# Performance work log

Measured on AMD Instinct MI355X. Metric: run time of the kernel, lower is better.

The kernel has to match this reference:

```python
import jax, jax.numpy as jnp
import numpy as np

B, T, D = 2, 4096, 1024
EI, N, DTR, K = 2048, 16, 64, 4  # d_inner, d_state, dt_rank, d_conv


def setup_inputs() -> dict:
    key = jax.random.key(0)
    ks = jax.random.split(key, 12)
    s = lambda k, shape, sc=0.02: jax.random.normal(k, shape, jnp.float32) * sc
    return dict(
        x=jax.random.normal(ks[0], (B, T, D), jnp.float32),
        W=s(ks[1], (B, D, D), 0.02),
        norm_w=jnp.ones((D,), jnp.float32),
        in_proj=s(ks[2], (2 * EI, D)),
        conv_w=s(ks[3], (EI, 1, K), 0.1),
        conv_b=jnp.zeros((EI,), jnp.float32),
        x_proj=s(ks[4], (DTR + 2 * N, EI)),
        dt_proj_w=s(ks[5], (EI, DTR), 0.1),
        dt_proj_b=jnp.full((EI,), -4.6, jnp.float32),  # softplus -> ~0.01 init dt
        A_log=jnp.log(jnp.tile(jnp.arange(1, N + 1, dtype=jnp.float32), (EI, 1))),
        D_param=jnp.ones((EI,), jnp.float32),
        out_proj=s(ks[6], (D, EI)),
        proj_write=s(ks[7], (D, D)),
        proj_read=s(ks[8], (D, D)),
        decay=jnp.float32(4.6),
    )


def _rmsnorm(x, w):
    return x * jax.lax.rsqrt(jnp.mean(x * x, axis=-1, keepdims=True) + 1e-6) * w


def _mamba(x, in_proj, conv_w, conv_b, x_proj, dt_proj_w, dt_proj_b, A_log, D_param, out_proj):
    # x: [B,T,D]
    xz = jnp.einsum('btd,ed->bte', x, in_proj)          # [B,T,2*EI]
    xp, z = jnp.split(xz, 2, axis=-1)
    # depthwise causal conv over time
    xc = jax.lax.conv_general_dilated(
        xp.transpose(0, 2, 1), conv_w, (1,), [(K - 1, 0)],
        dimension_numbers=('NCH', 'OIH', 'NCH'), feature_group_count=EI)
    xc = jax.nn.silu(xc.transpose(0, 2, 1) + conv_b)     # [B,T,EI]
    dbl = jnp.einsum('bte,fe->btf', xc, x_proj)          # [B,T,DTR+2N]
    dt = jax.nn.softplus(jnp.einsum('btr,er->bte', dbl[..., :DTR], dt_proj_w) + dt_proj_b)
    Bs = dbl[..., DTR:DTR + N]                           # [B,T,N]
    Cs = dbl[..., DTR + N:]                              # [B,T,N]
    A = -jnp.exp(A_log)                                  # [EI,N]

    def step(h, inp):
        dt_t, u_t, B_t, C_t = inp                        # [B,EI],[B,EI],[B,N],[B,N]
        dA = jnp.exp(dt_t[..., None] * A)                # [B,EI,N]
        h = dA * h + (dt_t * u_t)[..., None] * B_t[:, None, :]
        y = jnp.einsum('ben,bn->be', h, C_t)
        return h, y

    h0 = jnp.zeros((x.shape[0], EI, N), x.dtype)
    _, ys = jax.lax.scan(step, h0, (dt.transpose(1, 0, 2), xc.transpose(1, 0, 2),
                                    Bs.transpose(1, 0, 2), Cs.transpose(1, 0, 2)))
    y = ys.transpose(1, 0, 2) + xc * D_param
    y = y * jax.nn.silu(z)
    return jnp.einsum('bte,de->btd', y, out_proj)


def _memory_attend(out, W, proj_write, proj_read, decay):
    Bn, Tn, Dn = out.shape
    log_gamma = jnp.log(jax.nn.sigmoid(decay))
    v = jnp.einsum('btd,ed->bte', out, proj_write)       # [B,T,D]
    wk = jnp.pad(out[:, :-1], ((0, 0), (1, 0), (0, 0)))  # shift-right keys
    rk = out
    pos = jnp.arange(Tn)
    diffs = jnp.clip(pos[:, None] - 1 - pos[None, :], 0, None)
    M = jnp.exp(diffs * log_gamma) * (pos[:, None] > pos[None, :])  # [T,T] decay mask
    scores = jnp.einsum('btd,bsd->bts', rk, wk) * M      # [B,T,T]
    reads = jnp.einsum('bts,bsd->btd', scores, v)
    carry = jnp.einsum('bij,btj->bti', W, rk)
    reads = reads + carry * jnp.exp(pos * log_gamma)[None, :, None]
    out = out + 0.03 * jnp.einsum('btd,ed->bte', reads, proj_read)
    wvec = jnp.exp(jnp.arange(Tn - 1, -1, -1) * log_gamma)
    W_new = jnp.einsum('t,btd,bte->bde', wvec, v, wk) + jnp.exp(Tn * log_gamma) * W
    return out, W_new


def reference(x, W, norm_w, in_proj, conv_w, conv_b, x_proj, dt_proj_w, dt_proj_b,
              A_log, D_param, out_proj, proj_write, proj_read, decay):
    out = _mamba(_rmsnorm(x, norm_w), in_proj, conv_w, conv_b, x_proj,
                 dt_proj_w, dt_proj_b, A_log, D_param, out_proj)
    out, W_new = _memory_attend(out, W, proj_write, proj_read, decay)
    return x + out, W_new
```

## Files before the change

kernel.cpp:

```cpp
#include <hip/hip_runtime.h>
#include <cstdint>
#include <cstddef>

#define B_   2
#define T_   4096
#define D_   1024
#define EI_  2048
#define N_   16
#define KW_  4
#define NCH_ 128
#define CL_  32
#define CC_  512
#define NCC_ 8

typedef unsigned short ushort_t;
using bfrag = __attribute__((ext_vector_type(8))) short;
using f32x4 = __attribute__((ext_vector_type(4))) float;

__device__ __forceinline__ float bf2f(ushort_t u){
    union{ unsigned v; float f; } x; x.v = ((unsigned)u) << 16; return x.f;
}
__device__ __forceinline__ ushort_t f2bf(float f){
    union{ float f; unsigned v; } x; x.f = f;
    unsigned v = x.v;
    unsigned r = (v + 0x7FFFu + ((v >> 16) & 1u)) >> 16;
    return (ushort_t)r;
}
__device__ __forceinline__ void gl2lds16(const void* g, void* l){
    __builtin_amdgcn_global_load_lds((const __attribute__((address_space(1))) void*)g,
                                     (__attribute__((address_space(3))) void*)l, 16, 0, 0);
}

__global__ void cvtall_k(const float* __restrict__ ip, const float* __restrict__ op,
                         const float* __restrict__ pw, const float* __restrict__ pr,
                         const float* __restrict__ dtw,
                         ushort_t* __restrict__ ipW, ushort_t* __restrict__ opW,
                         ushort_t* __restrict__ pwW, ushort_t* __restrict__ prW,
                         ushort_t* __restrict__ dtwW){
    int i = blockIdx.x*256 + threadIdx.x;
    const float* src; ushort_t* dst; int off;
    if (i < 1048576)      { src = ip;  dst = ipW;  off = i; }
    else if (i < 1572864) { src = op;  dst = opW;  off = i - 1048576; }
    else if (i < 1835008) { src = pw;  dst = pwW;  off = i - 1572864; }
    else if (i < 2097152) { src = pr;  dst = prW;  off = i - 1835008; }
    else                  { src = dtw; dst = dtwW; off = i - 2097152; }
    float4 v = ((const float4*)src)[off];
    ushort4 o; o.x=f2bf(v.x); o.y=f2bf(v.y); o.z=f2bf(v.z); o.w=f2bf(v.w);
    ((ushort4*)dst)[off] = o;
}

__global__ void cvt_xproj_k(const float* __restrict__ w, ushort_t* __restrict__ out){
    int idx = blockIdx.x*256 + threadIdx.x;
    int row = idx >> 11, col = idx & 2047;
    out[idx] = (row < 96) ? f2bf(w[row*2048 + col]) : (ushort_t)0;
}

__global__ void convcst_k(const float* __restrict__ cw, float* __restrict__ cwT,
                          const float* __restrict__ decay, float* __restrict__ cst){
    int i = blockIdx.x*256 + threadIdx.x;
    if (i == 0) cst[0] = -log1pf(expf(-decay[0]));
    int e = i >> 2, k = i & 3;
    cwT[k*EI_ + e] = cw[i];
}

__global__ void rmsnorm_k(const float* __restrict__ x, const float* __restrict__ w,
                          ushort_t* __restrict__ xn){
    int row = blockIdx.x;
    int tid = threadIdx.x;
    const float* xr = x + (size_t)row * D_;
    float vals[4]; float s = 0.f;
#pragma unroll
    for (int i = 0; i < 4; i++){ vals[i] = xr[tid + i*256]; s += vals[i]*vals[i]; }
#pragma unroll
    for (int o = 1; o < 64; o <<= 1) s += __shfl_xor(s, o);
    __shared__ float red[4];
    if ((tid & 63) == 0) red[tid >> 6] = s;
    __syncthreads();
    float tot = red[0] + red[1] + red[2] + red[3];
    float sc = rsqrtf(tot / (float)D_ + 1e-6f);
    ushort_t* xo = xn + (size_t)row * D_;
#pragma unroll
    for (int i = 0; i < 4; i++) xo[tid + i*256] = f2bf(vals[i] * sc * w[tid + i*256]);
}

template<int EP, int TRI, int BAT>
__global__ void mgemm_k(const ushort_t* __restrict__ A, const ushort_t* __restrict__ Bw,
                        float* __restrict__ Cf, ushort_t* __restrict__ Cb,
                        const float* __restrict__ Cin, const float* __restrict__ cstp,
                        int M, int N, int K, int lda, int ldb, int ldc, int Nreal,
                        long sA, long sB, long sC, long sCin, long cA, long cB){
    __shared__ ushort_t As[128*64];
    __shared__ ushort_t Bs[128*64];
    int by = blockIdx.y;
    if (TRI == 2) by = gridDim.y - 1 - by;
    int m0 = by * 128, n0 = blockIdx.x * 128;
    if (TRI == 1 && n0 > m0) return;
    int bz = blockIdx.z;
    if (BAT == 1){
        int b = bz >> 3, c = bz & 7;
        A  += (size_t)b * sA + (size_t)c * cA;
        Bw += (size_t)b * sB + (size_t)c * cB;
    } else if (BAT == 2){
        A  += (size_t)bz * cA;
        Bw += (size_t)bz * cB;
    } else {
        A  += (size_t)bz * sA;
        Bw += (size_t)bz * sB;
    }
    if (Cf)  Cf  += (size_t)bz * sC;
    if (Cb)  Cb  += (size_t)bz * sC;
    if (Cin) Cin += (size_t)bz * sCin;

    int tid = threadIdx.x;
    int lane = tid & 63;
    int wv = tid >> 6;
    int wm = wv >> 1, wn = wv & 1;
    int l15 = lane & 15, l4 = lane >> 4;

    int Kend = (TRI == 2) ? (K < m0 + 128 ? K : m0 + 128) : K;

    f32x4 acc[4][4] = {};

    for (int k0 = 0; k0 < Kend; k0 += 64){
#pragma unroll
        for (int it = 0; it < 4; ++it){
            int q  = it*256 + tid;
            int r  = q >> 3;
            int cc = (q & 7) ^ (r & 7);
            const ushort_t* g = A + (size_t)(m0 + r)*lda + k0 + cc*8;
            gl2lds16((const void*)g, (void*)((char*)As + (q & ~63)*16));
        }
#pragma unroll
        for (int it = 0; it < 4; ++it){
            int q  = it*256 + tid;
            int r  = q >> 3;
            int cc = (q & 7) ^ (r & 7);
            const ushort_t* g = Bw + (size_t)(n0 + r)*ldb + k0 + cc*8;
            gl2lds16((const void*)g, (void*)((char*)Bs + (q & ~63)*16));
        }
        __syncthreads();
#pragma unroll
        for (int kh = 0; kh < 2; ++kh){
            bfrag av[4], bv[4];
#pragma unroll
            for (int i = 0; i < 4; i++){
                int row = wm*64 + i*16 + l15;
                int cc  = (l4 + kh*4) ^ (row & 7);
                av[i] = *(const bfrag*)(As + row*64 + cc*8);
                int rowb = wn*64 + i*16 + l15;
                int cb2  = (l4 + kh*4) ^ (rowb & 7);
                bv[i] = *(const bfrag*)(Bs + rowb*64 + cb2*8);
            }
#pragma unroll
            for (int i = 0; i < 4; i++)
#pragma unroll
                for (int j = 0; j < 4; j++)
                    acc[i][j] = __builtin_amdgcn_mfma_f32_16x16x32_bf16(av[i], bv[j], acc[i][j], 0, 0, 0);
        }
        __syncthreads();
    }

    float lg = (EP == 3 || EP == 10) ? cstp[0] : 0.f;
#pragma unroll
    for (int i = 0; i < 4; i++){
#pragma unroll
        for (int j = 0; j < 4; j++){
            int gmb = m0 + wm*64 + i*16 + l4*4;
            int gn  = n0 + wn*64 + j*16 + l15;
            if (gn >= Nreal) continue;
#pragma unroll
            for (int r = 0; r < 4; r++){
                int gm = gmb + r;
                float a = acc[i][j][r];
                size_t o = (size_t)gm*ldc + gn;
                if (EP == 0) Cf[o] = a;
                else if (EP == 1) Cb[o] = f2bf(a);
                else if (EP == 2){ Cf[o] = a; Cb[o] = f2bf(a); }
                else if (EP == 3){
                    float f = (gn < gm) ? __expf(lg * (float)(gm - 1 - gn)) : 0.f;
                    Cb[o] = f2bf(a * f);
                } else if (EP == 9){
                    Cf[o] = Cf[o] + 0.03f * a + Cin[o];
                } else if (EP == 10){
                    Cb[o] = f2bf(Cin[o] + __expf(lg * (float)gm) * a);
                }
            }
        }
    }
}

template<int EP, int TRI = 0, int BAT = 0>
static void mg(dim3 g, const ushort_t* A, const ushort_t* Bw, float* Cf, ushort_t* Cb,
               const float* Cin, const float* cstp, int M, int N, int K,
               int lda, int ldb, int ldc, int Nreal,
               long sA, long sB, long sC, long sCin, long cA, long cB, hipStream_t st){
    hipLaunchKernelGGL((mgemm_k<EP,TRI,BAT>), g, dim3(256), 0, st,
                       A, Bw, Cf, Cb, Cin, cstp, M, N, K, lda, ldb, ldc, Nreal,
                       sA, sB, sC, sCin, cA, cB);
}

__global__ void dblred_k(const float* __restrict__ part, float* __restrict__ dbl,
                         ushort_t* __restrict__ dbl_bf){
    int i = blockIdx.x*256 + threadIdx.x;
    if (i >= 8192*96) return;
    int r = i / 96, c = i - r*96;
    float s = 0.f;
#pragma unroll
    for (int k = 0; k < 4; k++) s += part[(size_t)k*8192*128 + (size_t)r*128 + c];
    dbl[i] = s;
    dbl_bf[i] = f2bf(s);
}

__global__ void conv_silu_k(const ushort_t* __restrict__ xpz, const float* __restrict__ cwT,
                            const float* __restrict__ cb, ushort_t* __restrict__ xc){
    int idx = blockIdx.x*256 + threadIdx.x;
    int e8 = (idx & 255) << 3;
    size_t bt = (size_t)(idx >> 8);
    int t = (int)(bt & (T_-1));
    float acc[8];
    float4 b0 = *(const float4*)&cb[e8], b1 = *(const float4*)&cb[e8+4];
    acc[0]=b0.x; acc[1]=b0.y; acc[2]=b0.z; acc[3]=b0.w;
    acc[4]=b1.x; acc[5]=b1.y; acc[6]=b1.z; acc[7]=b1.w;
#pragma unroll
    for (int k = 0; k < KW_; k++){
        int back = (KW_ - 1) - k;
        if (t >= back){
            const ushort_t* r = xpz + (bt - (size_t)back)*(size_t)(2*EI_) + e8;
            ushort4 u0 = *(const ushort4*)r, u1 = *(const ushort4*)(r + 4);
            float4 w0 = *(const float4*)&cwT[k*EI_ + e8];
            float4 w1 = *(const float4*)&cwT[k*EI_ + e8 + 4];
            acc[0] += w0.x*bf2f(u0.x); acc[1] += w0.y*bf2f(u0.y);
            acc[2] += w0.z*bf2f(u0.z); acc[3] += w0.w*bf2f(u0.w);
            acc[4] += w1.x*bf2f(u1.x); acc[5] += w1.y*bf2f(u1.y);
            acc[6] += w1.z*bf2f(u1.z); acc[7] += w1.w*bf2f(u1.w);
        }
    }
    ushort_t* o = xc + bt*EI_ + e8;
    ushort4 o0, o1;
#pragma unroll
    for (int q = 0; q < 4; q++){
        float a = acc[q];
        ((ushort_t*)&o0)[q] = f2bf(__fdividef(a, 1.f + __expf(-a)));
        float b = acc[4+q];
        ((ushort_t*)&o1)[q] = f2bf(__fdividef(b, 1.f + __expf(-b)));
    }
    *(ushort4*)o = o0; *(ushort4*)(o + 4) = o1;
}

__global__ void pass1_k(const ushort_t* __restrict__ dtb, const ushort_t* __restrict__ xcb,
                        const float* __restrict__ dbl, const float* __restrict__ dt_b,
                        float* __restrict__ hloc, float* __restrict__ sdt){
    __shared__ float BC[CL_][32];
    int bid = blockIdx.x;
    int eb = bid & 7, c = (bid >> 3) & (NCH_-1), b = bid >> 10;
    int tid = threadIdx.x;
    int e = eb*256 + tid;
    int t0 = c*CL_;
    for (int j = 0; j < 4; j++){
        int i = j*256 + tid;
        BC[i >> 5][i & 31] = dbl[((size_t)b*T_ + t0 + (i >> 5))*96 + 64 + (i & 31)];
    }
    __syncthreads();
    float bias = dt_b[e];
    float h[16];
#pragma unroll
    for (int n = 0; n < 16; n++) h[n] = 0.f;
    float s = 0.f;
    const ushort_t* drow = dtb + ((size_t)b*T_ + t0)*EI_;
    const ushort_t* urow = xcb + ((size_t)b*T_ + t0)*EI_;
    for (int i = 0; i < CL_; i++){
        float v2 = bf2f(drow[e]) + bias;
        float ev = __expf(-fabsf(v2));
        float tt = 1.f + ev;
        float dtv = fmaxf(v2, 0.f) + __logf(tt);
        float w1 = __fdividef((v2 > 0.f ? ev : 1.f), tt);
        float u = bf2f(urow[e]);
        float du = dtv * u;
        s += dtv;
        float w2 = w1*w1, w4 = w2*w2;
        float pw[4] = {w1, w2, w2*w1, w4};
        float4 Bq[4];
#pragma unroll
        for (int q = 0; q < 4; q++) Bq[q] = *(const float4*)&BC[i][q*4];
#pragma unroll
        for (int g = 0; g < 4; g++){
#pragma unroll
            for (int q = 0; q < 4; q++){
                int n = g*4 + q;
                h[n] = pw[q]*h[n] + du*((const float*)Bq)[n];
            }
            if (g < 3){
#pragma unroll
                for (int q = 0; q < 4; q++) pw[q] *= w4;
            }
        }
        drow += EI_; urow += EI_;
    }
    size_t base = ((size_t)(b*NCH_ + c)*16)*EI_ + e;
#pragma unroll
    for (int n = 0; n < 16; n++) hloc[base + (size_t)n*EI_] = h[n];
    sdt[(size_t)(b*NCH_ + c)*EI_ + e] = s;
}

__global__ void pass2_k(const float* __restrict__ hloc, const float* __restrict__ sdt,
                        float* __restrict__ hin){
    int idx = blockIdx.x*256 + threadIdx.x;
    int e = idx & (EI_-1), n = (idx >> 11) & 15, b = idx >> 15;
    float a = -(float)(n + 1);
    float h = 0.f;
    for (int c = 0; c < NCH_; c++){
        size_t o = ((size_t)(b*NCH_ + c)*16 + n)*EI_ + e;
        hin[o] = h;
        h = __expf(a * sdt[(size_t)(b*NCH_ + c)*EI_ + e])*h + hloc[o];
    }
}

__global__ void pass3_k(const ushort_t* __restrict__ dtb, const ushort_t* __restrict__ xcb,
                        const float* __restrict__ dbl, const float* __restrict__ dt_b,
                        const float* __restrict__ Dp, const ushort_t* __restrict__ xpz,
                        const float* __restrict__ hin, ushort_t* __restrict__ yb){
    __shared__ float BC[CL_][32];
    int bid = blockIdx.x;
    int eb = bid & 7, c = (bid >> 3) & (NCH_-1), b = bid >> 10;
    int tid = threadIdx.x;
    int e = eb*256 + tid;
    int t0 = c*CL_;
    for (int j = 0; j < 4; j++){
        int i = j*256 + tid;
        BC[i >> 5][i & 31] = dbl[((size_t)b*T_ + t0 + (i >> 5))*96 + 64 + (i & 31)];
    }
    __syncthreads();
    float bias = dt_b[e];
    float Dv = Dp[e];
    float h[16];
    size_t base = ((size_t)(b*NCH_ + c)*16)*EI_ + e;
#pragma unroll
    for (int n = 0; n < 16; n++) h[n] = hin[base + (size_t)n*EI_];
    const ushort_t* drow = dtb + ((size_t)b*T_ + t0)*EI_;
    const ushort_t* urow = xcb + ((size_t)b*T_ + t0)*EI_;
    const ushort_t* zrow = xpz + ((size_t)b*T_ + t0)*(size_t)(2*EI_) + EI_;
    ushort_t* yrow = yb + ((size_t)b*T_ + t0)*EI_;
    for (int i = 0; i < CL_; i++){
        float v2 = bf2f(drow[e]) + bias;
        float ev = __expf(-fabsf(v2));
        float tt = 1.f + ev;
        float dtv = fmaxf(v2, 0.f) + __logf(tt);
        float w1 = __fdividef((v2 > 0.f ? ev : 1.f), tt);
        float u = bf2f(urow[e]);
        float du = dtv * u;
        float w2 = w1*w1, w4 = w2*w2;
        float pw[4] = {w1, w2, w2*w1, w4};
        float4 Bq[4], Cq[4];
#pragma unroll
        for (int q = 0; q < 4; q++){ Bq[q] = *(const float4*)&BC[i][q*4];
                                     Cq[q] = *(const float4*)&BC[i][16+q*4]; }
        float ys4[4] = {0.f, 0.f, 0.f, 0.f};
#pragma unroll
        for (int g = 0; g < 4; g++){
#pragma unroll
            for (int q = 0; q < 4; q++){
                int n = g*4 + q;
                h[n] = pw[q]*h[n] + du*((const float*)Bq)[n];
                ys4[q] += h[n]*((const float*)Cq)[n];
            }
            if (g < 3){
#pragma unroll
                for (int q = 0; q < 4; q++) pw[q] *= w4;
            }
        }
        float ys = (ys4[0] + ys4[1]) + (ys4[2] + ys4[3]);
        float zz = bf2f(zrow[e]);
        float sil = __fdividef(zz, 1.f + __expf(-zz));
        yrow[e] = f2bf((ys + u*Dv) * sil);
        drow += EI_; urow += EI_; zrow += 2*EI_; yrow += EI_;
    }
}

__global__ void wkshift_k(const ushort_t* __restrict__ moutb, ushort_t* __restrict__ wk){
    size_t idx = (size_t)blockIdx.x*256 + threadIdx.x;
    int t = (int)((idx >> 10) & (T_-1));
    wk[idx] = (t == 0) ? (ushort_t)0 : moutb[idx - D_];
}

__global__ void wkTs_k(const ushort_t* __restrict__ in, ushort_t* __restrict__ out,
                       const float* __restrict__ cstp){
    __shared__ ushort_t tile[64][66];
    int bz = blockIdx.z;
    const ushort_t* ip = in + (size_t)bz*T_*D_;
    ushort_t* op = out + (size_t)bz*T_*D_;
    int c0 = blockIdx.x*64;
    int r0 = blockIdx.y*64;
    int cx = threadIdx.x & 63;
    int ry = threadIdx.x >> 6;
    float lg = cstp[0];
#pragma unroll
    for (int i = 0; i < 16; i++){
        int r = ry + i*4;
        tile[r][cx] = ip[(size_t)(r0 + r)*D_ + c0 + cx];
    }
    __syncthreads();
#pragma unroll
    for (int i = 0; i < 16; i++){
        int r = ry + i*4;
        int s = r0 + cx;
        float v = bf2f(tile[cx][r]) * __expf(lg * (float)(CC_ - 1 - (s & (CC_-1))));
        op[(size_t)(c0 + r)*T_ + r0 + cx] = f2bf(v);
    }
}

__global__ void prefix_k(const float* __restrict__ W, const ushort_t* __restrict__ ConTb,
                         const float* __restrict__ cstp,
                         ushort_t* __restrict__ Sdbf, float* __restrict__ out1){
    int i = blockIdx.x*256 + threadIdx.x;
    int b = i >> 18;
    int local4 = i & 262143;
    float gC = __expf(cstp[0] * (float)CC_);
    float4 s = ((const float4*)W)[i];
#pragma unroll
    for (int c = 0; c < NCC_; c++){
        size_t o4 = ((size_t)(b*NCC_ + c) << 18) + local4;
        ushort4 u; u.x=f2bf(s.x); u.y=f2bf(s.y); u.z=f2bf(s.z); u.w=f2bf(s.w);
        ((ushort4*)Sdbf)[o4] = u;
        ushort4 cc = ((const ushort4*)ConTb)[o4];
        s.x = gC*s.x + bf2f(cc.x); s.y = gC*s.y + bf2f(cc.y);
        s.z = gC*s.z + bf2f(cc.z); s.w = gC*s.w + bf2f(cc.w);
    }
    ((float4*)out1)[i] = s;
}

extern "C" void kernel_launch(void* const* d_in, const int* in_sizes, int n_in,
                              void* d_out, int out_size, void* d_ws, size_t ws_size,
                              hipStream_t stream){
    const float* x        = (const float*)d_in[0];
    const float* W        = (const float*)d_in[1];
    const float* norm_w   = (const float*)d_in[2];
    const float* in_proj  = (const float*)d_in[3];
    const float* conv_w   = (const float*)d_in[4];
    const float* conv_b   = (const float*)d_in[5];
    const float* x_proj   = (const float*)d_in[6];
    const float* dt_w     = (const float*)d_in[7];
    const float* dt_b     = (const float*)d_in[8];
    const float* A_log    = (const float*)d_in[9];  (void)A_log;
    const float* D_par    = (const float*)d_in[10];
    const float* out_proj = (const float*)d_in[11];
    const float* p_write  = (const float*)d_in[12];
    const float* p_read   = (const float*)d_in[13];
    const float* decay    = (const float*)d_in[14];

    const size_t MB = 1ull << 20;
    const size_t NEED = 232*MB;
    if (ws_size < NEED){
        hipMemsetAsync(d_out, 0, (size_t)out_size*sizeof(float), stream);
        return;
    }
    char* wsb = (char*)d_ws;
    ushort_t* ipW   = (ushort_t*)(wsb + 0);
    ushort_t* opW   = (ushort_t*)(wsb + 8*MB);
    ushort_t* pwW   = (ushort_t*)(wsb + 12*MB);
    ushort_t* prW   = (ushort_t*)(wsb + 14*MB);
    ushort_t* xpW   = (ushort_t*)(wsb + 16*MB);
    ushort_t* dtwW  = (ushort_t*)(wsb + 16*MB + 512*1024);
    float*    cstp  = (float*)   (wsb + 16*MB + 768*1024);
    float*    cwT   = (float*)   (wsb + 16*MB + 772*1024);
    float*    sdt   = (float*)   (wsb + 17*MB);
    float*    dbl   = (float*)   (wsb + 19*MB);
    ushort_t* dbl_bf= (ushort_t*)(wsb + 22*MB);
    ushort_t* xn_bf   = (ushort_t*)(wsb + 24*MB);
    ushort_t* mout_bf = (ushort_t*)(wsb + 24*MB);
    ushort_t* xc_bf = (ushort_t*)(wsb + 40*MB);
    ushort_t* ConTb = (ushort_t*)(wsb + 40*MB);
    ushort_t* dt_bf = (ushort_t*)(wsb + 72*MB);
    float*    reads = (float*)   (wsb + 72*MB);
    ushort_t* xpz   = (ushort_t*)(wsb + 104*MB);
    ushort_t* vT    = (ushort_t*)(wsb + 104*MB);
    ushort_t* wkTs  = (ushort_t*)(wsb + 120*MB);
    ushort_t* sc    = (ushort_t*)(wsb + 136*MB);
    ushort_t* reads_bf = (ushort_t*)(wsb + 144*MB);
    float*    hloc  = (float*)   (wsb + 168*MB);
    ushort_t* Sdbf  = (ushort_t*)(wsb + 168*MB);
    float*    dblpart = (float*) (wsb + 200*MB);
    float*    hin   = (float*)   (wsb + 200*MB);
    ushort_t* wk_bf = (ushort_t*)(wsb + 200*MB);
    ushort_t* y_bf  = (ushort_t*)(wsb + 168*MB);

    float* out0 = (float*)d_out;
    float* out1 = out0 + (size_t)B_*T_*D_;

    cvtall_k<<<8320, 256, 0, stream>>>(in_proj, out_proj, p_write, p_read, dt_w,
                                       ipW, opW, pwW, prW, dtwW);
    cvt_xproj_k<<<1024, 256, 0, stream>>>(x_proj, xpW);
    convcst_k<<<32, 256, 0, stream>>>(conv_w, cwT, decay, cstp);
    rmsnorm_k<<<B_*T_, 256, 0, stream>>>(x, norm_w, xn_bf);

    mg<1>(dim3(32,64,1), xn_bf, ipW, nullptr, xpz, nullptr, cstp,
          8192, 4096, 1024, 1024, 1024, 4096, 4096, 0,0,0,0,0,0, stream);
    conv_silu_k<<<(B_*T_*EI_)/(256*8), 256, 0, stream>>>(xpz, cwT, conv_b, xc_bf);
    mg<0,0,2>(dim3(1,64,4), xc_bf, xpW, dblpart, nullptr, nullptr, cstp,
          8192, 128, 512, 2048, 2048, 128, 128,
          0, 0, (long)8192*128, 0, 512, 512, stream);
    dblred_k<<<3072, 256, 0, stream>>>(dblpart, dbl, dbl_bf);
    mg<1>(dim3(16,64,1), dbl_bf, dtwW, nullptr, dt_bf, nullptr, cstp,
          8192, 2048, 64, 96, 64, 2048, 2048, 0,0,0,0,0,0, stream);

    pass1_k<<<B_*NCH_*8, 256, 0, stream>>>(dt_bf, xc_bf, dbl, dt_b, hloc, sdt);
    pass2_k<<<256, 256, 0, stream>>>(hloc, sdt, hin);
    pass3_k<<<B_*NCH_*8, 256, 0, stream>>>(dt_bf, xc_bf, dbl, dt_b, D_par,
                                           xpz, hin, y_bf);

    mg<2>(dim3(8,64,1), y_bf, opW, out0, mout_bf, nullptr, cstp,
          8192, 1024, 2048, 2048, 2048, 1024, 1024, 0,0,0,0,0,0, stream);

    mg<1>(dim3(32,8,2), pwW, mout_bf, nullptr, vT, nullptr, cstp,
          1024, 4096, 1024, 1024, 1024, 4096, 4096,
          0, (long)T_*D_, (long)D_*T_, 0, 0, 0, stream);
    wkshift_k<<<(B_*T_*D_)/256, 256, 0, stream>>>(mout_bf, wk_bf);
    wkTs_k<<<dim3(16,64,2), 256, 0, stream>>>(wk_bf, wkTs, cstp);

    mg<1,0,1>(dim3(8,8,16), vT, wkTs, nullptr, ConTb, nullptr, cstp,
          1024, 1024, 512, 4096, 4096, 1024, 1024,
          (long)D_*T_, (long)D_*T_, (long)D_*D_, 0, 512, 512, stream);

    prefix_k<<<2048, 256, 0, stream>>>(W, ConTb, cstp, Sdbf, out1);

    mg<3,1>(dim3(4,4,16), mout_bf, wk_bf, nullptr, sc, nullptr, cstp,
          512, 512, 1024, 1024, 1024, 512, 512,
          (long)CC_*D_, (long)CC_*D_, (long)CC_*CC_, 0, 0, 0, stream);
    mg<0,2,1>(dim3(8,4,16), sc, vT, reads, nullptr, nullptr, cstp,
          512, 1024, 512, 512, 4096, 1024, 1024,
          (long)NCC_*CC_*CC_, (long)D_*T_, (long)CC_*D_, 0,
          (long)CC_*CC_, 512, stream);
    mg<10>(dim3(8,4,16), mout_bf, Sdbf, nullptr, reads_bf, reads, cstp,
          512, 1024, 1024, 1024, 1024, 1024, 1024,
          (long)CC_*D_, (long)D_*D_, (long)CC_*D_, (long)CC_*D_, 0, 0, stream);

    mg<9>(dim3(8,64,1), reads_bf, prW, out0, nullptr, x, cstp,
          8192, 1024, 1024, 1024, 1024, 1024, 1024, 0,0,0, 0, 0, 0, stream);
}
```

Before: 556.6 us.

## Restructure chunked selective scan, drop wk shift buffer, and remap GEMM workgroups

The chunked scan now computes the local state and the intra-chunk output in pass1, writing the cumulative decay product and partial output in place into the dt and xc buffers. pass3 only applies the inter-chunk correction using powers of that cumulative product, and pass2 derives the chunk decay from it instead of a separate sum buffer. The shifted-key buffer is removed: the transpose kernel reads mout with a one-row offset, and the score GEMM takes mout_bf - D_ as its B operand, zeroing the affected column for the first chunk. GEMM workgroup IDs are also remapped in groups of eight, likely for cache locality, and packed float2 helpers are added. The risk is accuracy, because the cumulative decay is stored in bf16 and reconstructed with log/exp, and the negative pointer offset relies on masking to be correct.

```diff
diff --git a/kernel.cpp b/kernel.cpp
--- a/kernel.cpp
+++ b/kernel.cpp
@@ -29,6 +29,12 @@
 __device__ __forceinline__ void gl2lds16(const void* g, void* l){
     __builtin_amdgcn_global_load_lds((const __attribute__((address_space(1))) void*)g,
                                      (__attribute__((address_space(3))) void*)l, 16, 0, 0);
+}
+__device__ __forceinline__ float2 pkmul(float2 a, float2 b){
+    return make_float2(a.x*b.x, a.y*b.y);
+}
+__device__ __forceinline__ float2 pkfma(float2 a, float2 b, float2 c){
+    return make_float2(fmaf(a.x,b.x,c.x), fmaf(a.y,b.y,c.y));
 }
 
 __global__ void cvtall_k(const float* __restrict__ ip, const float* __restrict__ op,
@@ -91,9 +97,16 @@
                         long sA, long sB, long sC, long sCin, long cA, long cB){
     __shared__ ushort_t As[128*64];
     __shared__ ushort_t Bs[128*64];
-    int by = blockIdx.y;
-    if (TRI == 2) by = gridDim.y - 1 - by;
-    int m0 = by * 128, n0 = blockIdx.x * 128;
+    int gx = gridDim.x, gy = gridDim.y;
+    int bxi = blockIdx.x, byi = blockIdx.y;
+    int nwg = gx*gy;
+    if ((nwg & 7) == 0){
+        int id = byi*gx + bxi;
+        int q = nwg >> 3;
+        int id2 = (id & 7)*q + (id >> 3);
+        bxi = id2 % gx; byi = id2 / gx;
+    }
+    int m0 = byi * 128, n0 = bxi * 128;
     if (TRI == 1 && n0 > m0) return;
     int bz = blockIdx.z;
     if (BAT == 1){
@@ -177,7 +190,8 @@
                 else if (EP == 1) Cb[o] = f2bf(a);
                 else if (EP == 2){ Cf[o] = a; Cb[o] = f2bf(a); }
                 else if (EP == 3){
-                    float f = (gn < gm) ? __expf(lg * (float)(gm - 1 - gn)) : 0.f;
+                    bool zc = ((bz & 7) == 0) && (gn == 0);
+                    float f = (gn < gm && !zc) ? __expf(lg * (float)(gm - 1 - gn)) : 0.f;
                     Cb[o] = f2bf(a * f);
                 } else if (EP == 9){
                     Cf[o] = Cf[o] + 0.03f * a + Cin[o];
@@ -247,9 +261,9 @@
     *(ushort4*)o = o0; *(ushort4*)(o + 4) = o1;
 }
 
-__global__ void pass1_k(const ushort_t* __restrict__ dtb, const ushort_t* __restrict__ xcb,
+__global__ void pass1_k(ushort_t* __restrict__ dtb, ushort_t* __restrict__ xcb,
                         const float* __restrict__ dbl, const float* __restrict__ dt_b,
-                        float* __restrict__ hloc, float* __restrict__ sdt){
+                        const float* __restrict__ Dp, float* __restrict__ hloc){
     __shared__ float BC[CL_][32];
     int bid = blockIdx.x;
     int eb = bid & 7, c = (bid >> 3) & (NCH_-1), b = bid >> 10;
@@ -262,12 +276,13 @@
     }
     __syncthreads();
     float bias = dt_b[e];
-    float h[16];
-#pragma unroll
-    for (int n = 0; n < 16; n++) h[n] = 0.f;
-    float s = 0.f;
-    const ushort_t* drow = dtb + ((size_t)b*T_ + t0)*EI_;
-    const ushort_t* urow = xcb + ((size_t)b*T_ + t0)*EI_;
+    float Dv = Dp[e];
+    float2 h2[8];
+#pragma unroll
+    for (int q = 0; q < 8; q++) h2[q] = make_float2(0.f, 0.f);
+    float Pcum = 1.f;
+    ushort_t* drow = dtb + ((size_t)b*T_ + t0)*EI_;
+    ushort_t* urow = xcb + ((size_t)b*T_ + t0)*EI_;
     for (int i = 0; i < CL_; i++){
         float v2 = bf2f(drow[e]) + bias;
         float ev = __expf(-fabsf(v2));
@@ -276,117 +291,118 @@
         float w1 = __fdividef((v2 > 0.f ? ev : 1.f), tt);
         float u = bf2f(urow[e]);
         float du = dtv * u;
-        s += dtv;
-        float w2 = w1*w1, w4 = w2*w2;
-        float pw[4] = {w1, w2, w2*w1, w4};
-        float4 Bq[4];
-#pragma unroll
-        for (int q = 0; q < 4; q++) Bq[q] = *(const float4*)&BC[i][q*4];
-#pragma unroll
-        for (int g = 0; g < 4; g++){
-#pragma unroll
-            for (int q = 0; q < 4; q++){
-                int n = g*4 + q;
-                h[n] = pw[q]*h[n] + du*((const float*)Bq)[n];
-            }
-            if (g < 3){
-#pragma unroll
-                for (int q = 0; q < 4; q++) pw[q] *= w4;
-            }
-        }
+        Pcum *= w1;
+        drow[e] = f2bf(Pcum);
+        float w2 = w1*w1, w4 = w2*w2, w8 = w4*w4;
+        float2 w22 = make_float2(w2, w2), w42 = make_float2(w4, w4), w82 = make_float2(w8, w8);
+        float2 pw[8];
+        pw[0] = make_float2(w1, w2);
+        pw[1] = pkmul(pw[0], w22);
+        pw[2] = pkmul(pw[0], w42);
+        pw[3] = pkmul(pw[1], w42);
+        pw[4] = pkmul(pw[0], w82);
+        pw[5] = pkmul(pw[1], w82);
+        pw[6] = pkmul(pw[2], w82);
+        pw[7] = pkmul(pw[3], w82);
+        float2 du2 = make_float2(du, du);
+        float2 ysp[4];
+#pragma unroll
+        for (int q = 0; q < 4; q++) ysp[q] = make_float2(0.f, 0.f);
+#pragma unroll
+        for (int q = 0; q < 8; q++){
+            float2 B2 = *(const float2*)&BC[i][q*2];
+            float2 C2 = *(const float2*)&BC[i][16 + q*2];
+            h2[q] = pkfma(pw[q], h2[q], pkmul(du2, B2));
+            ysp[q & 3] = pkfma(h2[q], C2, ysp[q & 3]);
+        }
+        float ys = ((ysp[0].x + ysp[0].y) + (ysp[1].x + ysp[1].y))
+                 + ((ysp[2].x + ysp[2].y) + (ysp[3].x + ysp[3].y));
+        urow[e] = f2bf(ys + u*Dv);
         drow += EI_; urow += EI_;
     }
     size_t base = ((size_t)(b*NCH_ + c)*16)*EI_ + e;
 #pragma unroll
-    for (int n = 0; n < 16; n++) hloc[base + (size_t)n*EI_] = h[n];
-    sdt[(size_t)(b*NCH_ + c)*EI_ + e] = s;
-}
-
-__global__ void pass2_k(const float* __restrict__ hloc, const float* __restrict__ sdt,
+    for (int q = 0; q < 8; q++){
+        hloc[base + (size_t)(2*q)*EI_]   = h2[q].x;
+        hloc[base + (size_t)(2*q+1)*EI_] = h2[q].y;
+    }
+}
+
+__global__ void pass2_k(const float* __restrict__ hloc, const ushort_t* __restrict__ Pb,
                         float* __restrict__ hin){
     int idx = blockIdx.x*256 + threadIdx.x;
     int e = idx & (EI_-1), n = (idx >> 11) & 15, b = idx >> 15;
-    float a = -(float)(n + 1);
+    float np1 = (float)(n + 1);
     float h = 0.f;
     for (int c = 0; c < NCH_; c++){
         size_t o = ((size_t)(b*NCH_ + c)*16 + n)*EI_ + e;
         hin[o] = h;
-        h = __expf(a * sdt[(size_t)(b*NCH_ + c)*EI_ + e])*h + hloc[o];
-    }
-}
-
-__global__ void pass3_k(const ushort_t* __restrict__ dtb, const ushort_t* __restrict__ xcb,
-                        const float* __restrict__ dbl, const float* __restrict__ dt_b,
-                        const float* __restrict__ Dp, const ushort_t* __restrict__ xpz,
+        float Pfin = bf2f(Pb[((size_t)b*T_ + c*CL_ + CL_-1)*EI_ + e]);
+        float p = (Pfin > 0.f) ? __expf(np1 * __logf(Pfin)) : 0.f;
+        h = p*h + hloc[o];
+    }
+}
+
+__global__ void pass3_k(const ushort_t* __restrict__ Pb, const ushort_t* __restrict__ ylgb,
+                        const float* __restrict__ dbl, const ushort_t* __restrict__ xpz,
                         const float* __restrict__ hin, ushort_t* __restrict__ yb){
-    __shared__ float BC[CL_][32];
+    __shared__ float Cs[CL_][16];
     int bid = blockIdx.x;
     int eb = bid & 7, c = (bid >> 3) & (NCH_-1), b = bid >> 10;
     int tid = threadIdx.x;
     int e = eb*256 + tid;
     int t0 = c*CL_;
-    for (int j = 0; j < 4; j++){
+    for (int j = 0; j < 2; j++){
         int i = j*256 + tid;
-        BC[i >> 5][i & 31] = dbl[((size_t)b*T_ + t0 + (i >> 5))*96 + 64 + (i & 31)];
+        Cs[i >> 4][i & 15] = dbl[((size_t)b*T_ + t0 + (i >> 4))*96 + 80 + (i & 15)];
     }
     __syncthreads();
-    float bias = dt_b[e];
-    float Dv = Dp[e];
-    float h[16];
+    float2 h2[8];
     size_t base = ((size_t)(b*NCH_ + c)*16)*EI_ + e;
 #pragma unroll
-    for (int n = 0; n < 16; n++) h[n] = hin[base + (size_t)n*EI_];
-    const ushort_t* drow = dtb + ((size_t)b*T_ + t0)*EI_;
-    const ushort_t* urow = xcb + ((size_t)b*T_ + t0)*EI_;
-    const ushort_t* zrow = xpz + ((size_t)b*T_ + t0)*(size_t)(2*EI_) + EI_;
+    for (int q = 0; q < 8; q++){
+        h2[q].x = hin[base + (size_t)(2*q)*EI_];
+        h2[q].y = hin[base + (size_t)(2*q+1)*EI_];
+    }
+    const ushort_t* prow = Pb   + ((size_t)b*T_ + t0)*EI_;
+    const ushort_t* lrow = ylgb + ((size_t)b*T_ + t0)*EI_;
+    const ushort_t* zrow = xpz  + ((size_t)b*T_ + t0)*(size_t)(2*EI_) + EI_;
     ushort_t* yrow = yb + ((size_t)b*T_ + t0)*EI_;
     for (int i = 0; i < CL_; i++){
-        float v2 = bf2f(drow[e]) + bias;
-        float ev = __expf(-fabsf(v2));
-        float tt = 1.f + ev;
-        float dtv = fmaxf(v2, 0.f) + __logf(tt);
-        float w1 = __fdividef((v2 > 0.f ? ev : 1.f), tt);
-        float u = bf2f(urow[e]);
-        float du = dtv * u;
-        float w2 = w1*w1, w4 = w2*w2;
-        float pw[4] = {w1, w2, w2*w1, w4};
-        float4 Bq[4], Cq[4];
-#pragma unroll
-        for (int q = 0; q < 4; q++){ Bq[q] = *(const float4*)&BC[i][q*4];
-                                     Cq[q] = *(const float4*)&BC[i][16+q*4]; }
-        float ys4[4] = {0.f, 0.f, 0.f, 0.f};
-#pragma unroll
-        for (int g = 0; g < 4; g++){
-#pragma unroll
-            for (int q = 0; q < 4; q++){
-                int n = g*4 + q;
-                h[n] = pw[q]*h[n] + du*((const float*)Bq)[n];
-                ys4[q] += h[n]*((const float*)Cq)[n];
-            }
-            if (g < 3){
-#pragma unroll
-                for (int q = 0; q < 4; q++) pw[q] *= w4;
-            }
-        }
-        float ys = (ys4[0] + ys4[1]) + (ys4[2] + ys4[3]);
+        float P = bf2f(prow[e]);
+        float ylg = bf2f(lrow[e]);
         float zz = bf2f(zrow[e]);
+        float P2 = P*P, P4 = P2*P2, P8 = P4*P4;
+        float2 w22 = make_float2(P2, P2), w42 = make_float2(P4, P4), w82 = make_float2(P8, P8);
+        float2 pw[8];
+        pw[0] = make_float2(P, P2);
+        pw[1] = pkmul(pw[0], w22);
+        pw[2] = pkmul(pw[0], w42);
+        pw[3] = pkmul(pw[1], w42);
+        pw[4] = pkmul(pw[0], w82);
+        pw[5] = pkmul(pw[1], w82);
+        pw[6] = pkmul(pw[2], w82);
+        pw[7] = pkmul(pw[3], w82);
+        float2 csp[4];
+#pragma unroll
+        for (int q = 0; q < 4; q++) csp[q] = make_float2(0.f, 0.f);
+#pragma unroll
+        for (int q = 0; q < 8; q++){
+            float2 C2 = *(const float2*)&Cs[i][q*2];
+            csp[q & 3] = pkfma(pkmul(pw[q], h2[q]), C2, csp[q & 3]);
+        }
+        float corr = ((csp[0].x + csp[0].y) + (csp[1].x + csp[1].y))
+                   + ((csp[2].x + csp[2].y) + (csp[3].x + csp[3].y));
         float sil = __fdividef(zz, 1.f + __expf(-zz));
-        yrow[e] = f2bf((ys + u*Dv) * sil);
-        drow += EI_; urow += EI_; zrow += 2*EI_; yrow += EI_;
-    }
-}
-
-__global__ void wkshift_k(const ushort_t* __restrict__ moutb, ushort_t* __restrict__ wk){
-    size_t idx = (size_t)blockIdx.x*256 + threadIdx.x;
-    int t = (int)((idx >> 10) & (T_-1));
-    wk[idx] = (t == 0) ? (ushort_t)0 : moutb[idx - D_];
-}
-
-__global__ void wkTs_k(const ushort_t* __restrict__ in, ushort_t* __restrict__ out,
+        yrow[e] = f2bf((ylg + corr) * sil);
+        prow += EI_; lrow += EI_; zrow += 2*EI_; yrow += EI_;
+    }
+}
+
+__global__ void wkTs_k(const ushort_t* __restrict__ moutb, ushort_t* __restrict__ out,
                        const float* __restrict__ cstp){
     __shared__ ushort_t tile[64][66];
     int bz = blockIdx.z;
-    const ushort_t* ip = in + (size_t)bz*T_*D_;
     ushort_t* op = out + (size_t)bz*T_*D_;
     int c0 = blockIdx.x*64;
     int r0 = blockIdx.y*64;
@@ -396,7 +412,9 @@
 #pragma unroll
     for (int i = 0; i < 16; i++){
         int r = ry + i*4;
-        tile[r][cx] = ip[(size_t)(r0 + r)*D_ + c0 + cx];
+        int s = r0 + r;
+        tile[r][cx] = (s == 0) ? (ushort_t)0
+                    : moutb[((size_t)bz*T_ + s - 1)*D_ + c0 + cx];
     }
     __syncthreads();
 #pragma unroll
@@ -462,7 +480,6 @@
     ushort_t* dtwW  = (ushort_t*)(wsb + 16*MB + 512*1024);
     float*    cstp  = (float*)   (wsb + 16*MB + 768*1024);
     float*    cwT   = (float*)   (wsb + 16*MB + 772*1024);
-    float*    sdt   = (float*)   (wsb + 17*MB);
     float*    dbl   = (float*)   (wsb + 19*MB);
     ushort_t* dbl_bf= (ushort_t*)(wsb + 22*MB);
     ushort_t* xn_bf   = (ushort_t*)(wsb + 24*MB);
@@ -477,11 +494,10 @@
     ushort_t* sc    = (ushort_t*)(wsb + 136*MB);
     ushort_t* reads_bf = (ushort_t*)(wsb + 144*MB);
     float*    hloc  = (float*)   (wsb + 168*MB);
+    ushort_t* y_bf  = (ushort_t*)(wsb + 168*MB);
     ushort_t* Sdbf  = (ushort_t*)(wsb + 168*MB);
     float*    dblpart = (float*) (wsb + 200*MB);
     float*    hin   = (float*)   (wsb + 200*MB);
-    ushort_t* wk_bf = (ushort_t*)(wsb + 200*MB);
-    ushort_t* y_bf  = (ushort_t*)(wsb + 168*MB);
 
     float* out0 = (float*)d_out;
     float* out1 = out0 + (size_t)B_*T_*D_;
@@ -502,10 +518,9 @@
     mg<1>(dim3(16,64,1), dbl_bf, dtwW, nullptr, dt_bf, nullptr, cstp,
           8192, 2048, 64, 96, 64, 2048, 2048, 0,0,0,0,0,0, stream);
 
-    pass1_k<<<B_*NCH_*8, 256, 0, stream>>>(dt_bf, xc_bf, dbl, dt_b, hloc, sdt);
-    pass2_k<<<256, 256, 0, stream>>>(hloc, sdt, hin);
-    pass3_k<<<B_*NCH_*8, 256, 0, stream>>>(dt_bf, xc_bf, dbl, dt_b, D_par,
-                                           xpz, hin, y_bf);
+    pass1_k<<<B_*NCH_*8, 256, 0, stream>>>(dt_bf, xc_bf, dbl, dt_b, D_par, hloc);
+    pass2_k<<<256, 256, 0, stream>>>(hloc, dt_bf, hin);
+    pass3_k<<<B_*NCH_*8, 256, 0, stream>>>(dt_bf, xc_bf, dbl, xpz, hin, y_bf);
 
     mg<2>(dim3(8,64,1), y_bf, opW, out0, mout_bf, nullptr, cstp,
           8192, 1024, 2048, 2048, 2048, 1024, 1024, 0,0,0,0,0,0, stream);
@@ -513,8 +528,7 @@
     mg<1>(dim3(32,8,2), pwW, mout_bf, nullptr, vT, nullptr, cstp,
           1024, 4096, 1024, 1024, 1024, 4096, 4096,
           0, (long)T_*D_, (long)D_*T_, 0, 0, 0, stream);
-    wkshift_k<<<(B_*T_*D_)/256, 256, 0, stream>>>(mout_bf, wk_bf);
-    wkTs_k<<<dim3(16,64,2), 256, 0, stream>>>(wk_bf, wkTs, cstp);
+    wkTs_k<<<dim3(16,64,2), 256, 0, stream>>>(mout_bf, wkTs, cstp);
 
     mg<1,0,1>(dim3(8,8,16), vT, wkTs, nullptr, ConTb, nullptr, cstp,
           1024, 1024, 512, 4096, 4096, 1024, 1024,
@@ -522,7 +536,7 @@
 
     prefix_k<<<2048, 256, 0, stream>>>(W, ConTb, cstp, Sdbf, out1);
 
-    mg<3,1>(dim3(4,4,16), mout_bf, wk_bf, nullptr, sc, nullptr, cstp,
+    mg<3,1>(dim3(4,4,16), mout_bf, mout_bf - D_, nullptr, sc, nullptr, cstp,
           512, 512, 1024, 1024, 1024, 512, 512,
           (long)CC_*D_, (long)CC_*D_, (long)CC_*CC_, 0, 0, 0, stream);
     mg<0,2,1>(dim3(8,4,16), sc, vT, reads, nullptr, nullptr, cstp,
```

New measurement: 551.3 us. Within noise of the previous version (-1.0%).
